# Performance work log

Hardware: AMD Instinct MI355X
Metric: run time of the kernel (lower is better)

The kernel has to match this reference:

```python
import jax, jax.numpy as jnp
import numpy as np

B, T, V, D, DH, H = 4, 512, 32000, 768, 768, 4  # batch, seq, vocab, dim_in, dim_out(per-head & ffn), heads


def layer_norm(x, g, b, eps=1e-5):
    m = jnp.mean(x, axis=-1, keepdims=True)
    v = jnp.mean((x - m) ** 2, axis=-1, keepdims=True)
    return (x - m) * jax.lax.rsqrt(v + eps) * g + b


def setup_inputs() -> dict:
    key = jax.random.key(0)
    ks = jax.random.split(key, 20)
    s = 0.02
    f = lambda k, shp: (jax.random.normal(k, shp, jnp.float32) * s)
    return {
        "x": jax.random.randint(ks[0], (B, T), 0, V),
        "attention_mask": jax.random.randint(ks[1], (B, 1, T), 0, 2).astype(bool),
        "token_embed": f(ks[2], (V, D)),
        "segment_embed": f(ks[3], (V, D)),
        "ln_embed_g": jnp.ones((D,), jnp.float32), "ln_embed_b": jnp.zeros((D,), jnp.float32),
        "Wq": f(ks[4], (H, D, DH)), "bq": f(ks[5], (H, DH)),
        "Wk": f(ks[6], (H, D, DH)), "bk": f(ks[7], (H, DH)),
        "Wv": f(ks[8], (H, D, DH)), "bv": f(ks[9], (H, DH)),
        "Wo": f(ks[10], (H * DH, D)), "bo": f(ks[11], (D,)),
        "ln_attn_g": jnp.ones((D,), jnp.float32), "ln_attn_b": jnp.zeros((D,), jnp.float32),
        "W1": f(ks[12], (D, DH)), "b1": f(ks[13], (DH,)),
        "W2": f(ks[14], (DH, D)), "b2": f(ks[15], (D,)),
        "ln_enc_g": jnp.ones((D,), jnp.float32), "ln_enc_b": jnp.zeros((D,), jnp.float32),
        "Wproj": f(ks[16], (D, V)), "bproj": f(ks[17], (V,)),
        "Wcls": f(ks[18], (D, 2)), "bcls": f(ks[19], (2,)),
    }


def reference(x, attention_mask, token_embed, segment_embed, ln_embed_g, ln_embed_b,
              Wq, bq, Wk, bk, Wv, bv, Wo, bo, ln_attn_g, ln_attn_b,
              W1, b1, W2, b2, ln_enc_g, ln_enc_b, Wproj, bproj, Wcls, bcls):
    Bsz, Tlen = x.shape
    dim = token_embed.shape[1]
    # JointEmbedding: segment tensor is 0 for first half, 1 afterwards
    seg = jnp.zeros_like(x).at[:, Tlen // 2 + 1:].set(1)
    # positional encoding (faithful to source: exponent is 2*j/dim per column j,
    # sin on even columns, cos on odd columns, applied to pos/10000**exp)
    d = 2.0 * jnp.arange(dim, dtype=jnp.float32) / dim            # [D]
    p = jnp.arange(Tlen, dtype=jnp.float32)[:, None] / (10000.0 ** d)  # [T, D]
    pe = jnp.where(jnp.arange(dim) % 2 == 0, jnp.sin(p), jnp.cos(p))   # [T, D]
    emb = token_embed[x] + segment_embed[seg] + pe[None]          # [B, T, D]
    emb = layer_norm(emb, ln_embed_g, ln_embed_b)

    # Multi-head attention (vectorized over the per-head Python loop)
    Q = jnp.einsum('btd,hde->bhte', emb, Wq) + bq[None, :, None, :]
    K = jnp.einsum('btd,hde->bhte', emb, Wk) + bk[None, :, None, :]
    Vh = jnp.einsum('btd,hde->bhte', emb, Wv) + bv[None, :, None, :]
    # NOTE: source scales by seq_len**-0.5 (Q.size(1)), not head_dim**-0.5
    scores = jnp.einsum('bhte,bhse->bhts', Q, K) * (float(Tlen) ** -0.5)
    # NOTE: source masked_fill_'s with value 1e-9 (not -inf) before softmax
    scores = jnp.where(attention_mask[:, None, :, :], 1e-9, scores)
    attn = jax.nn.softmax(scores, axis=-1)
    ctx = jnp.einsum('bhts,bhse->bhte', attn, Vh)                 # [B, H, T, DH]
    cat = ctx.transpose(0, 2, 1, 3).reshape(Bsz, Tlen, -1)        # head concat order
    attn_out = layer_norm(cat @ Wo + bo, ln_attn_g, ln_attn_b)

    # FFN (no residual in source; dropout is identity at inference)
    h = jax.nn.gelu(attn_out @ W1 + b1, approximate=False)
    enc = layer_norm(h @ W2 + b2, ln_enc_g, ln_enc_b)

    token_pred = enc @ Wproj + bproj                              # [B, T, V]
    logits = jax.nn.log_softmax(token_pred, axis=-1)
    cls_out = enc[:, 0, :] @ Wcls + bcls                          # [B, 2]
    return logits, cls_out
```

## Files before the change

kernel.cpp:

```cpp
#include <hip/hip_runtime.h>
#include <hip/hip_bf16.h>
#include <stdint.h>

#define B_ 4
#define T_ 512
#define V_ 32000
#define D_ 768
#define DH_ 768
#define H_ 4
#define R_ 2048

typedef unsigned short u16;
typedef __attribute__((ext_vector_type(4))) float f32x4;
typedef __attribute__((ext_vector_type(8))) short s16x8;
typedef __attribute__((ext_vector_type(8))) unsigned short u16x8;
typedef __attribute__((address_space(3))) char* lds_cp;
typedef const __attribute__((address_space(1))) char* gl_cp;

__device__ __forceinline__ float bf2f(u16 u){
  union { float f; unsigned int i; } w; w.i = ((unsigned int)u) << 16; return w.f;
}
__device__ __forceinline__ u16 f2bf(float f){
  union { float f; unsigned int i; } w; w.f = f;
  unsigned int r = w.i + 0x7fffu + ((w.i >> 16) & 1u);
  return (u16)(r >> 16);
}

__device__ __forceinline__ float block_sum(float v, float* red){
  #pragma unroll
  for (int o = 32; o; o >>= 1) v += __shfl_down(v, o);
  __syncthreads();
  if ((threadIdx.x & 63) == 0) red[threadIdx.x >> 6] = v;
  __syncthreads();
  return red[0] + red[1] + red[2] + red[3];
}
__device__ __forceinline__ float block_max(float v, float* red){
  #pragma unroll
  for (int o = 32; o; o >>= 1) v = fmaxf(v, __shfl_down(v, o));
  __syncthreads();
  if ((threadIdx.x & 63) == 0) red[threadIdx.x >> 6] = v;
  __syncthreads();
  return fmaxf(fmaxf(red[0], red[1]), fmaxf(red[2], red[3]));
}

__global__ void mask_convert(const void* __restrict__ mraw, int* __restrict__ mout){
  __shared__ int isbyte;
  if (threadIdx.x == 0) isbyte = 0;
  __syncthreads();
  const unsigned char* by = (const unsigned char*)mraw;
  int f = 0;
  for (int i = threadIdx.x; i < 2048; i += 256)
    if ((i & 3) && by[i]) f = 1;
  if (f) atomicOr(&isbyte, 1);
  __syncthreads();
  if (isbyte){
    for (int i = threadIdx.x; i < 2048; i += 256) mout[i] = by[i] ? 1 : 0;
  } else {
    const int* mi = (const int*)mraw;
    for (int i = threadIdx.x; i < 2048; i += 256) mout[i] = mi[i] ? 1 : 0;
  }
}

__global__ __launch_bounds__(256)
void transpose_all(const float* __restrict__ Wq, const float* __restrict__ Wk,
                   const float* __restrict__ Wv, const float* __restrict__ Wo,
                   const float* __restrict__ W1, const float* __restrict__ W2,
                   u16* __restrict__ wqT, u16* __restrict__ wkT,
                   u16* __restrict__ wvT, u16* __restrict__ woT,
                   u16* __restrict__ w1T, u16* __restrict__ w2T){
  __shared__ u16 tile[32][33];
  int z = blockIdx.z;
  const float* in; u16* out; int out_ld = 768;
  if (z < 4)      { in = Wq + (long)z * 589824;        out = wqT + (long)z * 589824; }
  else if (z < 8) { int k = z - 4;  in = Wk + (long)k * 589824; out = wkT + (long)k * 589824; }
  else if (z < 12){ int k = z - 8;  in = Wv + (long)k * 589824; out = wvT + (long)k * 589824; }
  else if (z < 16){ int k = z - 12; in = Wo + (long)k * 589824; out = woT + (long)k * 768; out_ld = 3072; }
  else if (z == 16){ in = W1; out = w1T; }
  else             { in = W2; out = w2T; }
  int c0 = blockIdx.x * 32, r0 = blockIdx.y * 32;
  int tx = threadIdx.x & 31, ty = threadIdx.x >> 5;
  #pragma unroll
  for (int i = 0; i < 32; i += 8)
    tile[ty + i][tx] = f2bf(in[(long)(r0 + ty + i) * 768 + (c0 + tx)]);
  __syncthreads();
  #pragma unroll
  for (int i = 0; i < 32; i += 8)
    out[(long)(c0 + ty + i) * out_ld + (r0 + tx)] = tile[tx][ty + i];
}

__global__ __launch_bounds__(256)
void transpose_f2b(const float* __restrict__ in, u16* __restrict__ out, int R, int C){
  __shared__ u16 tile[32][33];
  int c0 = blockIdx.x * 32, r0 = blockIdx.y * 32;
  int tx = threadIdx.x & 31, ty = threadIdx.x >> 5;
  #pragma unroll
  for (int i = 0; i < 32; i += 8)
    tile[ty + i][tx] = f2bf(in[(long)(r0 + ty + i) * C + (c0 + tx)]);
  __syncthreads();
  #pragma unroll
  for (int i = 0; i < 32; i += 8)
    out[(long)(c0 + ty + i) * R + (r0 + tx)] = tile[tx][ty + i];
}

__global__ __launch_bounds__(256)
void embed_ln(const int* __restrict__ x, const float* __restrict__ tok,
              const float* __restrict__ seg, const float* __restrict__ g,
              const float* __restrict__ bb, u16* __restrict__ emb){
  __shared__ float red[4];
  int r = blockIdx.x, t = r & 511;
  int tid = threadIdx.x;
  long trow = (long)x[r] * D_;
  long srow = (t > 256) ? (long)D_ : 0;
  float v[3];
  float s = 0.f;
  #pragma unroll
  for (int q = 0; q < 3; ++q){
    int j = tid + q * 256;
    float d = (2.0f * (float)j) * (1.0f / 768.0f);
    float p = (float)t * powf(10000.0f, -d);
    float pe = (j & 1) ? cosf(p) : sinf(p);
    v[q] = tok[trow + j] + seg[srow + j] + pe;
    s += v[q];
  }
  float mean = block_sum(s, red) * (1.0f / 768.0f);
  float vs = 0.f;
  #pragma unroll
  for (int q = 0; q < 3; ++q){ float dd = v[q] - mean; vs += dd * dd; }
  float var = block_sum(vs, red) * (1.0f / 768.0f);
  float inv = rsqrtf(var + 1e-5f);
  #pragma unroll
  for (int q = 0; q < 3; ++q){
    int j = tid + q * 256;
    emb[(long)r * D_ + j] = f2bf((v[q] - mean) * inv * g[j] + bb[j]);
  }
}

__global__ __launch_bounds__(256)
void ln_rows(const u16* __restrict__ in, const float* __restrict__ g,
             const float* __restrict__ bb, u16* __restrict__ out){
  __shared__ float red[4];
  long r = blockIdx.x;
  int tid = threadIdx.x;
  const u16* row = in + r * D_;
  float v[3];
  float s = 0.f;
  #pragma unroll
  for (int q = 0; q < 3; ++q){ v[q] = bf2f(row[tid + q * 256]); s += v[q]; }
  float mean = block_sum(s, red) * (1.0f / 768.0f);
  float vs = 0.f;
  #pragma unroll
  for (int q = 0; q < 3; ++q){ float dd = v[q] - mean; vs += dd * dd; }
  float var = block_sum(vs, red) * (1.0f / 768.0f);
  float inv = rsqrtf(var + 1e-5f);
  #pragma unroll
  for (int q = 0; q < 3; ++q){
    int j = tid + q * 256;
    out[r * D_ + j] = f2bf((v[q] - mean) * inv * g[j] + bb[j]);
  }
}

__global__ __launch_bounds__(256)
void attn_softmax(u16* __restrict__ S, const int* __restrict__ mask){
  __shared__ float red[4];
  int t = blockIdx.x, z = blockIdx.y, b = z >> 2;
  u16* row = S + (long)z * (T_ * T_) + (long)t * T_;
  int tid = threadIdx.x;
  int s0 = tid, s1 = tid + 256;
  float v0 = mask[b * T_ + s0] ? 1e-9f : bf2f(row[s0]);
  float v1 = mask[b * T_ + s1] ? 1e-9f : bf2f(row[s1]);
  float mx = block_max(fmaxf(v0, v1), red);
  float e0 = expf(v0 - mx), e1 = expf(v1 - mx);
  float l = block_sum(e0 + e1, red);
  float inv = 1.0f / l;
  row[s0] = f2bf(e0 * inv);
  row[s1] = f2bf(e1 * inv);
}

__global__ __launch_bounds__(256)
void lsm_b2f(const u16* __restrict__ pred, float* __restrict__ out){
  __shared__ float sm[256], sl[256];
  long r = blockIdx.x;
  const u16x8* rv = (const u16x8*)(pred + r * (long)V_);
  int tid = threadIdx.x;
  float m = -1e30f, l = 0.f;
  for (int c = tid; c < V_ / 8; c += 256){
    u16x8 v = rv[c];
    #pragma unroll
    for (int j = 0; j < 8; ++j){
      float x = bf2f(v[j]);
      if (x > m){ l = l * expf(m - x) + 1.0f; m = x; }
      else l += expf(x - m);
    }
  }
  sm[tid] = m; sl[tid] = l;
  __syncthreads();
  #pragma unroll
  for (int s = 128; s; s >>= 1){
    if (tid < s){
      float m2 = sm[tid + s], l2 = sl[tid + s];
      float M = fmaxf(sm[tid], m2);
      sl[tid] = sl[tid] * expf(sm[tid] - M) + l2 * expf(m2 - M);
      sm[tid] = M;
    }
    __syncthreads();
  }
  float lse = sm[0] + logf(sl[0]);
  f32x4* orow = (f32x4*)(out + r * (long)V_);
  for (int c = tid; c < V_ / 8; c += 256){
    u16x8 v = rv[c];
    f32x4 o0, o1;
    #pragma unroll
    for (int j = 0; j < 4; ++j){ o0[j] = bf2f(v[j]) - lse; o1[j] = bf2f(v[j + 4]) - lse; }
    orow[2 * c] = o0; orow[2 * c + 1] = o1;
  }
}

__global__ __launch_bounds__(256)
void log_softmax_rows(float* __restrict__ tp){
  __shared__ float sm[256], sl[256];
  long r = blockIdx.x;
  float* row = tp + r * (long)V_;
  f32x4* rv = (f32x4*)row;
  int tid = threadIdx.x;
  float m = -1e30f, l = 0.f;
  for (int c = tid; c < V_ / 4; c += 256){
    f32x4 v = rv[c];
    #pragma unroll
    for (int j = 0; j < 4; ++j){
      float x = v[j];
      if (x > m){ l = l * expf(m - x) + 1.0f; m = x; }
      else l += expf(x - m);
    }
  }
  sm[tid] = m; sl[tid] = l;
  __syncthreads();
  #pragma unroll
  for (int s = 128; s; s >>= 1){
    if (tid < s){
      float m2 = sm[tid + s], l2 = sl[tid + s];
      float M = fmaxf(sm[tid], m2);
      sl[tid] = sl[tid] * expf(sm[tid] - M) + l2 * expf(m2 - M);
      sm[tid] = M;
    }
    __syncthreads();
  }
  float lse = sm[0] + logf(sl[0]);
  for (int c = tid; c < V_ / 4; c += 256){
    f32x4 v = rv[c];
    #pragma unroll
    for (int j = 0; j < 4; ++j) v[j] -= lse;
    rv[c] = v;
  }
}

__global__ __launch_bounds__(256)
void cls_head(const u16* __restrict__ enc, const float* __restrict__ Wc,
              const float* __restrict__ bc, float* __restrict__ out){
  int w = threadIdx.x >> 6, lane = threadIdx.x & 63;
  const u16* e = enc + (long)w * (T_ * D_);
  float a0 = 0.f, a1 = 0.f;
  for (int k = lane; k < D_; k += 64){
    float ev = bf2f(e[k]);
    a0 += ev * Wc[k * 2 + 0];
    a1 += ev * Wc[k * 2 + 1];
  }
  #pragma unroll
  for (int o = 32; o; o >>= 1){ a0 += __shfl_down(a0, o); a1 += __shfl_down(a1, o); }
  if (lane == 0){
    out[(long)B_ * T_ * V_ + w * 2 + 0] = a0 + bc[0];
    out[(long)B_ * T_ * V_ + w * 2 + 1] = a1 + bc[1];
  }
}

template<int GELU, int F32OUT>
__global__ __launch_bounds__(256, 2)
void gemm_bt(const u16* __restrict__ A, const u16* __restrict__ Bt,
             const float* __restrict__ bias, void* __restrict__ Cv,
             int lda, int ldb,
             long sAzb, long sAzh, long sBzb, long sBzh, long sbz,
             long sCzb, long sCzh, long sCb, long sCr, long sCc,
             int zsh, float scale, int nt){
  extern __shared__ char smem[];
  u16* sA = (u16*)smem;
  u16* sB = sA + 2 * 128 * 64;
  int tid = threadIdx.x, lane = tid & 63, wid = tid >> 6;
  int wm = wid >> 1, wn = wid & 1;
  int lrow = lane & 15, lquad = lane >> 4;

  unsigned gx = gridDim.x, gy = gridDim.y;
  unsigned nwg = gx * gy * gridDim.z;
  unsigned id = blockIdx.x + gx * (blockIdx.y + gy * blockIdx.z);
  unsigned qq = nwg >> 3, rr = nwg & 7, xcd = id & 7, loc = id >> 3;
  unsigned nid = (xcd < rr ? xcd * (qq + 1) : rr * (qq + 1) + (xcd - rr) * qq) + loc;
  unsigned bx = nid % gx, tmpq = nid / gx;
  unsigned by = tmpq % gy, bz = tmpq / gy;

  int z = (int)bz, zb = z >> zsh, zh = z & ((1 << zsh) - 1);
  long bm = (long)bx * 128, bn = (long)by * 128;
  const u16* Az = A + zb * sAzb + zh * sAzh;
  const u16* Bz = Bt + zb * sBzb + zh * sBzh;

  f32x4 acc[4][4] = {};

  auto stage = [&](int buf, int kt){
    #pragma unroll
    for (int q = 0; q < 4; ++q){
      int seg = wid * 4 + q;
      int idx = seg * 64 + lane;
      int r = idx >> 3, c = idx & 7;
      int ksw = (c ^ (r & 7)) << 3;
      const u16* srcA = Az + (bm + r) * lda + kt * 64 + ksw;
      const u16* srcB = Bz + (bn + r) * ldb + kt * 64 + ksw;
      __builtin_amdgcn_global_load_lds((gl_cp)srcA,
          (lds_cp)((char*)(sA + buf * 8192) + seg * 1024), 16, 0, 0);
      __builtin_amdgcn_global_load_lds((gl_cp)srcB,
          (lds_cp)((char*)(sB + buf * 8192) + seg * 1024), 16, 0, 0);
    }
  };

  stage(0, 0);
  __syncthreads();
  int cur = 0;
  for (int t = 0; t < nt; ++t){
    if (t + 1 < nt) stage(cur ^ 1, t + 1);
    const u16* a0 = sA + cur * 8192;
    const u16* b0 = sB + cur * 8192;
    #pragma unroll
    for (int kk = 0; kk < 2; ++kk){
      int koff = (((kk * 4 + lquad) ^ (lrow & 7)) << 3);
      s16x8 af[4], bfv[4];
      #pragma unroll
      for (int m = 0; m < 4; ++m)
        af[m] = *(const s16x8*)(a0 + (wm * 64 + m * 16 + lrow) * 64 + koff);
      #pragma unroll
      for (int n = 0; n < 4; ++n)
        bfv[n] = *(const s16x8*)(b0 + (wn * 64 + n * 16 + lrow) * 64 + koff);
      #pragma unroll
      for (int m = 0; m < 4; ++m)
        #pragma unroll
        for (int n = 0; n < 4; ++n)
          acc[m][n] = __builtin_amdgcn_mfma_f32_16x16x32_bf16(af[m], bfv[n], acc[m][n], 0, 0, 0);
    }
    __syncthreads();
    cur ^= 1;
  }

  long czbase = zb * sCzb + zh * sCzh;
  #pragma unroll
  for (int n = 0; n < 4; ++n){
    long col = bn + wn * 64 + n * 16 + lrow;
    float bv = bias ? bias[zb * sbz + col] : 0.f;
    #pragma unroll
    for (int m = 0; m < 4; ++m){
      #pragma unroll
      for (int j = 0; j < 4; ++j){
        long row = bm + wm * 64 + m * 16 + lquad * 4 + j;
        float v = acc[m][n][j] * scale + bv;
        if (GELU) v = 0.5f * v * (1.0f + erff(v * 0.70710678118654752f));
        long ci = czbase + (row >> 9) * sCb + (row & 511) * sCr + col * sCc;
        if (F32OUT) ((float*)Cv)[ci] = v;
        else        ((u16*)Cv)[ci] = f2bf(v);
      }
    }
  }
}

template<int F32OUT>
__global__ __launch_bounds__(512, 2)
void gemm8p(const u16* __restrict__ A, const u16* __restrict__ Bt,
            const float* __restrict__ bias, void* __restrict__ Cv){
  __shared__ char smem[131072];
  const int tid = threadIdx.x, lane = tid & 63, wid = tid >> 6;
  const int wm = wid >> 2, wn = wid & 3;
  const int lrow = lane & 15, lquad = lane >> 4;

  unsigned id = blockIdx.x + 8u * blockIdx.y;
  unsigned wg = (id & 7u) * 125u + (id >> 3);
  const long bm = (long)(wg & 7u) * 256;
  const long bn = (long)(wg >> 3) * 256;
  const int NT = 24;

  f32x4 acc[8][4] = {};

  auto stage_half = [&](int k, int kind, int h){
    int slot = k & 3;
    int r = tid >> 2, c = tid & 3;
    int lc = c ^ ((r >> 1) & 3);
    const u16* src = (kind ? Bt + (bn + h * 128 + r) * 768
                           : A  + (bm + h * 128 + r) * 768) + k * 32 + lc * 8;
    char* dst = smem + slot * 32768 + kind * 16384 + h * 8192 + (wid * 64) * 16;
    __builtin_amdgcn_global_load_lds((gl_cp)src, (lds_cp)dst, 16, 0, 0);
  };
  const int ksw = (lquad ^ ((lrow >> 1) & 3)) * 16;
  auto aBaseOf = [&](int k){ return smem + (k & 3) * 32768 + wm * 8192; };
  auto bBaseOf = [&](int k){
    return smem + (k & 3) * 32768 + 16384 + (wn >> 1) * 8192 + ((wn & 1) * 64) * 64;
  };

  #pragma unroll
  for (int k = 0; k < 3; ++k){
    stage_half(k, 0, 0); stage_half(k, 0, 1);
    stage_half(k, 1, 0); stage_half(k, 1, 1);
  }
  asm volatile("s_waitcnt vmcnt(4)" ::: "memory");
  __builtin_amdgcn_s_barrier();
  __builtin_amdgcn_sched_barrier(0);

  s16x8 af0[4], bfv[4];
  {
    const char* aB = aBaseOf(0); const char* bB = bBaseOf(0);
    #pragma unroll
    for (int nf = 0; nf < 4; ++nf)
      bfv[nf] = *(const s16x8*)(bB + (nf * 16 + lrow) * 64 + ksw);
    #pragma unroll
    for (int mf = 0; mf < 4; ++mf)
      af0[mf] = *(const s16x8*)(aB + (mf * 16 + lrow) * 64 + ksw);
  }
  asm volatile("s_waitcnt lgkmcnt(0)" ::: "memory");
  __builtin_amdgcn_sched_barrier(0);

  for (int k = 0; k < NT; ++k){
    const char* aB = aBaseOf(k);
    if (k + 3 < NT){
      stage_half(k + 3, 0, 0); stage_half(k + 3, 0, 1);
      stage_half(k + 3, 1, 0); stage_half(k + 3, 1, 1);
    }
    s16x8 af1[4];
    #pragma unroll
    for (int mf = 0; mf < 4; ++mf)
      af1[mf] = *(const s16x8*)(aB + ((mf + 4) * 16 + lrow) * 64 + ksw);
    __builtin_amdgcn_sched_barrier(0);
    __builtin_amdgcn_s_setprio(1);
    #pragma unroll
    for (int mf = 0; mf < 4; ++mf)
      #pragma unroll
      for (int nf = 0; nf < 4; ++nf)
        acc[mf][nf] = __builtin_amdgcn_mfma_f32_16x16x32_bf16(af0[mf], bfv[nf], acc[mf][nf], 0, 0, 0);
    __builtin_amdgcn_s_setprio(0);
    __builtin_amdgcn_sched_barrier(0);
    asm volatile("s_waitcnt lgkmcnt(0)" ::: "memory");
    __builtin_amdgcn_sched_barrier(0);
    s16x8 afn[4], bfn[4];
    if (k + 1 < NT){
      const char* aN = aBaseOf(k + 1); const char* bN = bBaseOf(k + 1);
      #pragma unroll
      for (int nf = 0; nf < 4; ++nf)
        bfn[nf] = *(const s16x8*)(bN + (nf * 16 + lrow) * 64 + ksw);
      #pragma unroll
      for (int mf = 0; mf < 4; ++mf)
        afn[mf] = *(const s16x8*)(aN + (mf * 16 + lrow) * 64 + ksw);
    }
    __builtin_amdgcn_sched_barrier(0);
    __builtin_amdgcn_s_setprio(1);
    #pragma unroll
    for (int mf = 0; mf < 4; ++mf)
      #pragma unroll
      for (int nf = 0; nf < 4; ++nf)
        acc[mf + 4][nf] = __builtin_amdgcn_mfma_f32_16x16x32_bf16(af1[mf], bfv[nf], acc[mf + 4][nf], 0, 0, 0);
    __builtin_amdgcn_s_setprio(0);
    __builtin_amdgcn_sched_barrier(0);
    asm volatile("s_waitcnt lgkmcnt(0)" ::: "memory");
    __builtin_amdgcn_sched_barrier(0);
    if (k <= NT - 4)      { asm volatile("s_waitcnt vmcnt(4)" ::: "memory"); }
    else if (k == NT - 3) { asm volatile("s_waitcnt vmcnt(0)" ::: "memory"); }
    __builtin_amdgcn_s_barrier();
    __builtin_amdgcn_sched_barrier(0);
    #pragma unroll
    for (int i = 0; i < 4; ++i){ af0[i] = afn[i]; bfv[i] = bfn[i]; }
  }

  #pragma unroll
  for (int nf = 0; nf < 4; ++nf){
    long col = bn + wn * 64 + nf * 16 + lrow;
    float bv = bias[col];
    #pragma unroll
    for (int mf = 0; mf < 8; ++mf){
      #pragma unroll
      for (int j = 0; j < 4; ++j){
        long row = bm + wm * 128 + mf * 16 + lquad * 4 + j;
        float v = acc[mf][nf][j] + bv;
        if (F32OUT) ((float*)Cv)[row * (long)V_ + col] = v;
        else        ((u16*)Cv)[row * (long)V_ + col] = f2bf(v);
      }
    }
  }
}

extern "C" void kernel_launch(void* const* d_in, const int* in_sizes, int n_in,
                              void* d_out, int out_size, void* d_ws, size_t ws_size,
                              hipStream_t stream){
  const int*   x     = (const int*)d_in[0];
  const void*  amask = d_in[1];
  const float* tok = (const float*)d_in[2];
  const float* seg = (const float*)d_in[3];
  const float* lng = (const float*)d_in[4];
  const float* lnb = (const float*)d_in[5];
  const float* Wq  = (const float*)d_in[6];
  const float* bq  = (const float*)d_in[7];
  const float* Wk  = (const float*)d_in[8];
  const float* bk  = (const float*)d_in[9];
  const float* Wv  = (const float*)d_in[10];
  const float* bv  = (const float*)d_in[11];
  const float* Wo  = (const float*)d_in[12];
  const float* bo  = (const float*)d_in[13];
  const float* lag = (const float*)d_in[14];
  const float* lab = (const float*)d_in[15];
  const float* W1  = (const float*)d_in[16];
  const float* b1  = (const float*)d_in[17];
  const float* W2  = (const float*)d_in[18];
  const float* b2  = (const float*)d_in[19];
  const float* leg = (const float*)d_in[20];
  const float* leb = (const float*)d_in[21];
  const float* Wp  = (const float*)d_in[22];
  const float* bp  = (const float*)d_in[23];
  const float* Wc  = (const float*)d_in[24];
  const float* bc  = (const float*)d_in[25];
  float* out = (float*)d_out;
  char* ws = (char*)d_ws;

  size_t off = 0;
  auto alloc = [&](size_t bytes){ size_t o = off; off += (bytes + 255) & ~(size_t)255; return o; };
  size_t o_mask = alloc(2048 * 4);
  size_t o_emb  = alloc((size_t)R_ * D_ * 2);
  size_t o_wqT  = alloc((size_t)H_ * D_ * DH_ * 2);
  size_t o_wkT  = alloc((size_t)H_ * D_ * DH_ * 2);
  size_t o_wvT  = alloc((size_t)H_ * D_ * DH_ * 2);
  size_t o_woT  = alloc((size_t)3072 * 768 * 2);
  size_t o_w1T  = alloc((size_t)768 * 768 * 2);
  size_t o_w2T  = alloc((size_t)768 * 768 * 2);
  size_t o_Q    = alloc((size_t)B_ * H_ * T_ * DH_ * 2);
  size_t o_K    = alloc((size_t)B_ * H_ * T_ * DH_ * 2);
  size_t o_VT   = alloc((size_t)B_ * H_ * DH_ * T_ * 2);
  size_t o_S    = alloc((size_t)B_ * H_ * T_ * T_ * 2);
  size_t o_cat  = alloc((size_t)R_ * 3072 * 2);
  size_t o_ap   = alloc((size_t)R_ * D_ * 2);
  size_t o_ao   = alloc((size_t)R_ * D_ * 2);
  size_t o_h1   = alloc((size_t)R_ * D_ * 2);
  size_t o_ep   = alloc((size_t)R_ * D_ * 2);
  size_t o_enc  = alloc((size_t)R_ * D_ * 2);
  size_t o_wpT  = o_Q;
  size_t off_base = off;
  size_t o_pred = alloc((size_t)R_ * V_ * 2);
  int bigws = (ws_size >= off);
  if (ws_size < off_base) return;

  int* maskI = (int*)(ws + o_mask);
  u16* emb  = (u16*)(ws + o_emb);
  u16* wqT  = (u16*)(ws + o_wqT);
  u16* wkT  = (u16*)(ws + o_wkT);
  u16* wvT  = (u16*)(ws + o_wvT);
  u16* woT  = (u16*)(ws + o_woT);
  u16* w1T  = (u16*)(ws + o_w1T);
  u16* w2T  = (u16*)(ws + o_w2T);
  u16* Qb   = (u16*)(ws + o_Q);
  u16* Kb   = (u16*)(ws + o_K);
  u16* VTb  = (u16*)(ws + o_VT);
  u16* Sb   = (u16*)(ws + o_S);
  u16* catb = (u16*)(ws + o_cat);
  u16* apb  = (u16*)(ws + o_ap);
  u16* aob  = (u16*)(ws + o_ao);
  u16* h1b  = (u16*)(ws + o_h1);
  u16* epb  = (u16*)(ws + o_ep);
  u16* encb = (u16*)(ws + o_enc);
  u16* wpT  = (u16*)(ws + o_wpT);
  u16* predb = (u16*)(ws + o_pred);

  const long sQK_zb = (long)H_ * T_ * DH_;
  const long sQK_zh = (long)T_ * DH_;

  mask_convert<<<1, 256, 0, stream>>>(amask, maskI);
  transpose_all<<<dim3(24, 24, 18), 256, 0, stream>>>(Wq, Wk, Wv, Wo, W1, W2,
      wqT, wkT, wvT, woT, w1T, w2T);
  embed_ln<<<R_, 256, 0, stream>>>(x, tok, seg, lng, lnb, emb);

  gemm_bt<0,0><<<dim3(16, 6, 4), 256, 65536, stream>>>(emb, wqT, bq, Qb,
      768, 768, 0, 0, (long)768 * 768, 0, 768,
      sQK_zh, 0, sQK_zb, 768, 1, 0, 1.0f, 12);
  gemm_bt<0,0><<<dim3(16, 6, 4), 256, 65536, stream>>>(emb, wkT, bk, Kb,
      768, 768, 0, 0, (long)768 * 768, 0, 768,
      sQK_zh, 0, sQK_zb, 768, 1, 0, 1.0f, 12);
  gemm_bt<0,0><<<dim3(16, 6, 4), 256, 65536, stream>>>(emb, wvT, bv, VTb,
      768, 768, 0, 0, (long)768 * 768, 0, 768,
      sQK_zh, 0, sQK_zb, 1, 512, 0, 1.0f, 12);

  gemm_bt<0,0><<<dim3(4, 4, 16), 256, 65536, stream>>>(Qb, Kb, nullptr, Sb,
      768, 768, sQK_zb, sQK_zh, sQK_zb, sQK_zh, 0,
      (long)H_ * T_ * T_, (long)T_ * T_, 0, 512, 1, 2, 0.044194173824159216f, 12);

  attn_softmax<<<dim3(512, 16), 256, 0, stream>>>(Sb, maskI);

  gemm_bt<0,0><<<dim3(4, 6, 16), 256, 65536, stream>>>(Sb, VTb, nullptr, catb,
      512, 512, (long)H_ * T_ * T_, (long)T_ * T_, sQK_zb, sQK_zh, 0,
      (long)T_ * 3072, 768, 0, 3072, 1, 2, 1.0f, 8);

  gemm_bt<0,0><<<dim3(16, 6, 1), 256, 65536, stream>>>(catb, woT, bo, apb,
      3072, 3072, 0, 0, 0, 0, 0,
      0, 0, (long)512 * 768, 768, 1, 0, 1.0f, 48);
  ln_rows<<<R_, 256, 0, stream>>>(apb, lag, lab, aob);

  gemm_bt<1,0><<<dim3(16, 6, 1), 256, 65536, stream>>>(aob, w1T, b1, h1b,
      768, 768, 0, 0, 0, 0, 0,
      0, 0, (long)512 * 768, 768, 1, 0, 1.0f, 12);
  gemm_bt<0,0><<<dim3(16, 6, 1), 256, 65536, stream>>>(h1b, w2T, b2, epb,
      768, 768, 0, 0, 0, 0, 0,
      0, 0, (long)512 * 768, 768, 1, 0, 1.0f, 12);
  ln_rows<<<R_, 256, 0, stream>>>(epb, leg, leb, encb);

  transpose_f2b<<<dim3(1000, 24, 1), 256, 0, stream>>>(Wp, wpT, 768, 32000);

  if (bigws){
    gemm8p<0><<<dim3(8, 125), 512, 0, stream>>>(encb, wpT, bp, predb);
    lsm_b2f<<<R_, 256, 0, stream>>>(predb, out);
  } else {
    gemm8p<1><<<dim3(8, 125), 512, 0, stream>>>(encb, wpT, bp, out);
    log_softmax_rows<<<R_, 256, 0, stream>>>(out);
  }
  cls_head<<<1, 256, 0, stream>>>(encb, Wc, bc, out);

  (void)in_sizes; (void)n_in; (void)out_size;
}
```

Measured before the change: 498.7 us.

## Fuse per-panel row max/sum-exp into projection GEMM epilogue for log-softmax

The vocab projection GEMM epilogue now computes a per-row running max and sum of exponentials for each 256-column panel, using a wave shuffle reduction followed by an LDS reduction. It writes these partial stats to a small workspace buffer. The log-softmax kernel merges the 125 panel stats per row instead of re-reading the whole bf16 logits row, which removes one full pass over the 2048x32000 prediction matrix. In exchange the GEMM epilogue does extra expf, shuffles and a block barrier, and the stats come from fp32 values before bf16 rounding, so they differ slightly from the stored logits.

```diff
diff --git a/kernel.cpp b/kernel.cpp
--- a/kernel.cpp
+++ b/kernel.cpp
@@ -177,20 +177,15 @@
 }
 
 __global__ __launch_bounds__(256)
-void lsm_b2f(const u16* __restrict__ pred, float* __restrict__ out){
+void lsm_single(const u16* __restrict__ pred, const float2* __restrict__ rowstat,
+                float* __restrict__ out){
   __shared__ float sm[256], sl[256];
   long r = blockIdx.x;
-  const u16x8* rv = (const u16x8*)(pred + r * (long)V_);
   int tid = threadIdx.x;
   float m = -1e30f, l = 0.f;
-  for (int c = tid; c < V_ / 8; c += 256){
-    u16x8 v = rv[c];
-    #pragma unroll
-    for (int j = 0; j < 8; ++j){
-      float x = bf2f(v[j]);
-      if (x > m){ l = l * expf(m - x) + 1.0f; m = x; }
-      else l += expf(x - m);
-    }
+  if (tid < 125){
+    float2 st = rowstat[r * 128 + tid];
+    m = st.x; l = st.y;
   }
   sm[tid] = m; sl[tid] = l;
   __syncthreads();
@@ -205,6 +200,7 @@
     __syncthreads();
   }
   float lse = sm[0] + logf(sl[0]);
+  const u16x8* rv = (const u16x8*)(pred + r * (long)V_);
   f32x4* orow = (f32x4*)(out + r * (long)V_);
   for (int c = tid; c < V_ / 8; c += 256){
     u16x8 v = rv[c];
@@ -368,7 +364,8 @@
 template<int F32OUT>
 __global__ __launch_bounds__(512, 2)
 void gemm8p(const u16* __restrict__ A, const u16* __restrict__ Bt,
-            const float* __restrict__ bias, void* __restrict__ Cv){
+            const float* __restrict__ bias, void* __restrict__ Cv,
+            float2* __restrict__ rowstat){
   __shared__ char smem[131072];
   const int tid = threadIdx.x, lane = tid & 63, wid = tid >> 6;
   const int wm = wid >> 2, wn = wid & 3;
@@ -469,19 +466,60 @@
     for (int i = 0; i < 4; ++i){ af0[i] = afn[i]; bfv[i] = bfn[i]; }
   }
 
-  #pragma unroll
-  for (int nf = 0; nf < 4; ++nf){
-    long col = bn + wn * 64 + nf * 16 + lrow;
-    float bv = bias[col];
-    #pragma unroll
-    for (int mf = 0; mf < 8; ++mf){
-      #pragma unroll
-      for (int j = 0; j < 4; ++j){
-        long row = bm + wm * 128 + mf * 16 + lquad * 4 + j;
-        float v = acc[mf][nf][j] + bv;
-        if (F32OUT) ((float*)Cv)[row * (long)V_ + col] = v;
-        else        ((u16*)Cv)[row * (long)V_ + col] = f2bf(v);
+  float bvv[4];
+  #pragma unroll
+  for (int nf = 0; nf < 4; ++nf)
+    bvv[nf] = bias[bn + wn * 64 + nf * 16 + lrow];
+
+  float* sredm = (float*)smem;
+  float* sredl = sredm + 1024;
+
+  #pragma unroll
+  for (int mf = 0; mf < 8; ++mf){
+    #pragma unroll
+    for (int j = 0; j < 4; ++j){
+      long row = bm + wm * 128 + mf * 16 + lquad * 4 + j;
+      float v[4];
+      #pragma unroll
+      for (int nf = 0; nf < 4; ++nf){
+        v[nf] = acc[mf][nf][j] + bvv[nf];
+        long col = bn + wn * 64 + nf * 16 + lrow;
+        if (F32OUT) ((float*)Cv)[row * (long)V_ + col] = v[nf];
+        else        ((u16*)Cv)[row * (long)V_ + col] = f2bf(v[nf]);
       }
+      if (!F32OUT){
+        float mx = fmaxf(fmaxf(v[0], v[1]), fmaxf(v[2], v[3]));
+        float sme = expf(v[0] - mx) + expf(v[1] - mx) + expf(v[2] - mx) + expf(v[3] - mx);
+        #pragma unroll
+        for (int o = 1; o < 16; o <<= 1){
+          float mo = __shfl_xor(mx, o);
+          float so = __shfl_xor(sme, o);
+          float M = fmaxf(mx, mo);
+          sme = sme * expf(mx - M) + so * expf(mo - M);
+          mx = M;
+        }
+        if (lrow == 0){
+          int rl = wm * 128 + mf * 16 + lquad * 4 + j;
+          sredm[wn * 256 + rl] = mx;
+          sredl[wn * 256 + rl] = sme;
+        }
+      }
+    }
+  }
+  if (!F32OUT){
+    __syncthreads();
+    if (tid < 256){
+      float mx = sredm[tid], l = sredl[tid];
+      #pragma unroll
+      for (int w = 1; w < 4; ++w){
+        float m2 = sredm[w * 256 + tid], l2 = sredl[w * 256 + tid];
+        float M = fmaxf(mx, m2);
+        l = l * expf(mx - M) + l2 * expf(m2 - M);
+        mx = M;
+      }
+      int panel = (int)(wg >> 3);
+      float2 st; st.x = mx; st.y = l;
+      rowstat[(bm + tid) * 128 + panel] = st;
     }
   }
 }
@@ -521,6 +559,7 @@
   size_t off = 0;
   auto alloc = [&](size_t bytes){ size_t o = off; off += (bytes + 255) & ~(size_t)255; return o; };
   size_t o_mask = alloc(2048 * 4);
+  size_t o_rows = alloc((size_t)R_ * 128 * 8);
   size_t o_emb  = alloc((size_t)R_ * D_ * 2);
   size_t o_wqT  = alloc((size_t)H_ * D_ * DH_ * 2);
   size_t o_wkT  = alloc((size_t)H_ * D_ * DH_ * 2);
@@ -545,6 +584,7 @@
   if (ws_size < off_base) return;
 
   int* maskI = (int*)(ws + o_mask);
+  float2* rowstat = (float2*)(ws + o_rows);
   u16* emb  = (u16*)(ws + o_emb);
   u16* wqT  = (u16*)(ws + o_wqT);
   u16* wkT  = (u16*)(ws + o_wkT);
@@ -609,10 +649,10 @@
   transpose_f2b<<<dim3(1000, 24, 1), 256, 0, stream>>>(Wp, wpT, 768, 32000);
 
   if (bigws){
-    gemm8p<0><<<dim3(8, 125), 512, 0, stream>>>(encb, wpT, bp, predb);
-    lsm_b2f<<<R_, 256, 0, stream>>>(predb, out);
+    gemm8p<0><<<dim3(8, 125), 512, 0, stream>>>(encb, wpT, bp, predb, rowstat);
+    lsm_single<<<R_, 256, 0, stream>>>(predb, rowstat, out);
   } else {
-    gemm8p<1><<<dim3(8, 125), 512, 0, stream>>>(encb, wpT, bp, out);
+    gemm8p<1><<<dim3(8, 125), 512, 0, stream>>>(encb, wpT, bp, out, nullptr);
     log_softmax_rows<<<R_, 256, 0, stream>>>(out);
   }
   cls_head<<<1, 256, 0, stream>>>(encb, Wc, bc, out);
```

After: 532.0 us. 1.07x slower.
